# Performance work log

Hardware: AMD Instinct MI355X
Metric: run time of the kernel (lower is better)

## Reference

```python
import jax, jax.numpy as jnp
import numpy as np

# 256 graphs x 1024 nodes, 64 channels, 4.19M edges (avg degree 16)
B, N, C, E = 256, 1024, 64, 4194304
RATIO = 0.5
K = 512  # ceil(RATIO * N), fixed per-graph keep count


def setup_inputs() -> dict:
    key = jax.random.key(0)
    k1, k2, k3, k4, k5, k6 = jax.random.split(key, 6)
    x = jax.random.normal(k1, (B * N, C), jnp.float32)
    w = jax.random.normal(k2, (1, C), jnp.float32) / np.sqrt(C)  # score_layer.weight
    b = jnp.zeros((1,), jnp.float32)                              # score_layer.bias
    # edges sampled within each graph so filter_adj semantics are realistic
    g = jax.random.randint(k3, (E,), 0, B)
    src = jax.random.randint(k4, (E,), 0, N)
    dst = jax.random.randint(k5, (E,), 0, N)
    edge_index = jnp.stack([g * N + src, g * N + dst]).astype(jnp.int32)
    edge_attr = jax.random.normal(k6, (E,), jnp.float32)
    batch = jnp.repeat(jnp.arange(B, dtype=jnp.int32), N)  # nondecreasing graph ids
    return {"x": x, "w": w, "b": b, "edge_index": edge_index,
            "edge_attr": edge_attr, "batch": batch}


def reference(x, w, b, edge_index, edge_attr, batch):
    # scores = Linear(x).squeeze() / ||W||  (bias also divided, as in source)
    scores = (x @ w.T + b)[:, 0] / jnp.linalg.norm(w)  # [B*N]
    # per-graph ratio top-k (equal-size graphs -> dense [B, N] top_k, fixed K)
    _, top_idx = jax.lax.top_k(scores.reshape(B, N), K)          # [B, K] local ids
    perm = (top_idx + (jnp.arange(B) * N)[:, None]).reshape(-1)  # [B*K] global ids
    x_p = x[perm]          # gather surviving node features
    batch_p = batch[perm]
    # filter_adj: relabel kept nodes 0..B*K-1, drop edges touching removed nodes.
    # For jit-able static shapes we keep [2, E] and mask dropped edges to -1
    # instead of compacting (mask returned for downstream compaction).
    new_idx = jnp.full((B * N,), -1, jnp.int32).at[perm].set(
        jnp.arange(B * K, dtype=jnp.int32))
    r = new_idx[edge_index[0]]
    c = new_idx[edge_index[1]]
    mask = (r >= 0) & (c >= 0)
    ei = jnp.where(mask, jnp.stack([r, c]), -1)
    ea = jnp.where(mask, edge_attr, jnp.zeros((), edge_attr.dtype))
    return x_p, ei, ea, batch_p, scores, perm, mask
```

## Files before the change

### kernel.cpp

```cpp
#include <hip/hip_runtime.h>
#include <math.h>

#define BGRAPHS 256
#define NNODES  1024
#define CCH     64
#define NEDGE   4194304
#define KKEEP   512

typedef unsigned long long u64;
typedef unsigned int u32;
typedef unsigned short u16;
typedef float  f32x4 __attribute__((ext_vector_type(4)));
typedef int    i32x4 __attribute__((ext_vector_type(4)));

#define OFF_XP   0
#define OFF_EI0  8388608
#define OFF_EI1  (8388608 + NEDGE)
#define OFF_EA   16777216
#define OFF_BP   20971520
#define OFF_SC   21102592
#define OFF_PM   21364736
#define OFF_MSK  21495808

#define EDGE_BLOCKS   2048
#define GATHER_BLOCKS 8192

__global__ __launch_bounds__(256) void score_kernel(
    const float* __restrict__ x, const float* __restrict__ w,
    const float* __restrict__ bias, float* __restrict__ sco)
{
    __shared__ float s_w[CCH];
    const int tid = threadIdx.x;
    if (tid < CCH) s_w[tid] = w[tid];
    __syncthreads();

    double n2 = 0.0;
    #pragma unroll
    for (int k = 0; k < CCH; ++k) { double v = (double)s_w[k]; n2 += v * v; }
    const float nrm = (float)sqrt(n2);
    const float bv = bias[0];

    const int node = blockIdx.x * 256 + tid;
    const f32x4* x4 = (const f32x4*)x;
    double acc = 0.0;
    #pragma unroll
    for (int k = 0; k < 16; ++k) {
        f32x4 xv = x4[node * 16 + k];
        acc += (double)xv.x * (double)s_w[4 * k + 0];
        acc += (double)xv.y * (double)s_w[4 * k + 1];
        acc += (double)xv.z * (double)s_w[4 * k + 2];
        acc += (double)xv.w * (double)s_w[4 * k + 3];
    }
    sco[node] = ((float)acc + bv) / nrm;
}

__device__ __forceinline__ u64 cmpex(u64 key, int j, bool dir, int tid) {
    u64 o = (u64)__shfl_xor((long long)key, j, 64);
    bool lower = ((tid & j) == 0);
    u64 mn = key < o ? key : o;
    u64 mx = key < o ? o : key;
    return (dir == lower) ? mn : mx;
}

__global__ __launch_bounds__(1024) void sort_kernel(
    const float* __restrict__ sco, const int* __restrict__ batch,
    float* __restrict__ pmo, float* __restrict__ bpo,
    u16* __restrict__ table16, u16* __restrict__ src16)
{
    __shared__ u64 s_key[NNODES];
    const int b = blockIdx.x;
    const int tid = threadIdx.x;
    const int node = b * NNODES + tid;

    const float score = sco[node];
    u32 u = __float_as_uint(score);
    u32 mu = u ^ (u32)(((int)u >> 31) | 0x80000000);
    u64 key = ((u64)(~mu) << 32) | (u32)tid;

    #pragma unroll
    for (int k = 2; k <= 64; k <<= 1) {
        bool dir = ((tid & k) == 0);
        for (int j = k >> 1; j > 0; j >>= 1)
            key = cmpex(key, j, dir, tid);
    }
    s_key[tid] = key;

    for (int k = 128; k <= NNODES; k <<= 1) {
        bool dir = ((tid & k) == 0);
        for (int j = k >> 1; j >= 64; j >>= 1) {
            __syncthreads();
            int ixj = tid ^ j;
            if (ixj > tid) {
                u64 a = s_key[tid], c = s_key[ixj];
                if ((a > c) == dir) { s_key[tid] = c; s_key[ixj] = a; }
            }
        }
        __syncthreads();
        key = s_key[tid];
        #pragma unroll
        for (int j = 32; j > 0; j >>= 1)
            key = cmpex(key, j, dir, tid);
        s_key[tid] = key;
    }

    const int lidx = (int)(u32)key;
    const int g = b * NNODES + lidx;
    if (tid < KKEEP) {
        pmo[b * KKEEP + tid] = (float)g;
        bpo[b * KKEEP + tid] = (float)batch[g];
        table16[g] = (u16)tid;
        src16[b * KKEEP + tid] = (u16)lidx;
    } else {
        table16[g] = 0xFFFFu;
    }
}

__global__ __launch_bounds__(256) void edge_gather_kernel(
    const int* __restrict__ ei, const float* __restrict__ ea,
    const u16* __restrict__ table16,
    const float* __restrict__ x, const u16* __restrict__ src16,
    float* __restrict__ ei0o, float* __restrict__ ei1o,
    float* __restrict__ eao, float* __restrict__ msk,
    float* __restrict__ xp)
{
    const int tid = threadIdx.x;
    if (blockIdx.x < EDGE_BLOCKS) {
        const int i0 = blockIdx.x * 512 + tid;
        const int i1 = i0 + 256;
        const i32x4* s4p = (const i32x4*)ei;
        const i32x4* d4p = (const i32x4*)(ei + NEDGE);
        const f32x4* a4p = (const f32x4*)ea;

        i32x4 sA = __builtin_nontemporal_load(&s4p[i0]);
        i32x4 sB = __builtin_nontemporal_load(&s4p[i1]);
        i32x4 dA = __builtin_nontemporal_load(&d4p[i0]);
        i32x4 dB = __builtin_nontemporal_load(&d4p[i1]);
        f32x4 aA = __builtin_nontemporal_load(&a4p[i0]);
        f32x4 aB = __builtin_nontemporal_load(&a4p[i1]);

        u16 vsA[4], vdA[4], vsB[4], vdB[4];
        #pragma unroll
        for (int q = 0; q < 4; ++q) vsA[q] = table16[((const int*)&sA)[q]];
        #pragma unroll
        for (int q = 0; q < 4; ++q) vdA[q] = table16[((const int*)&dA)[q]];
        #pragma unroll
        for (int q = 0; q < 4; ++q) vsB[q] = table16[((const int*)&sB)[q]];
        #pragma unroll
        for (int q = 0; q < 4; ++q) vdB[q] = table16[((const int*)&dB)[q]];

        f32x4 rA, cA, oA, mA, rB, cB, oB, mB;
        #pragma unroll
        for (int q = 0; q < 4; ++q) {
            {
                int m = (vsA[q] != 0xFFFFu) && (vdA[q] != 0xFFFFu);
                int r = ((((const int*)&sA)[q] >> 10) << 9) + (int)vsA[q];
                int c = ((((const int*)&dA)[q] >> 10) << 9) + (int)vdA[q];
                ((float*)&rA)[q] = m ? (float)r : -1.0f;
                ((float*)&cA)[q] = m ? (float)c : -1.0f;
                ((float*)&oA)[q] = m ? ((const float*)&aA)[q] : 0.0f;
                ((float*)&mA)[q] = (float)m;
            }
            {
                int m = (vsB[q] != 0xFFFFu) && (vdB[q] != 0xFFFFu);
                int r = ((((const int*)&sB)[q] >> 10) << 9) + (int)vsB[q];
                int c = ((((const int*)&dB)[q] >> 10) << 9) + (int)vdB[q];
                ((float*)&rB)[q] = m ? (float)r : -1.0f;
                ((float*)&cB)[q] = m ? (float)c : -1.0f;
                ((float*)&oB)[q] = m ? ((const float*)&aB)[q] : 0.0f;
                ((float*)&mB)[q] = (float)m;
            }
        }

        __builtin_nontemporal_store(rA, &((f32x4*)ei0o)[i0]);
        __builtin_nontemporal_store(rB, &((f32x4*)ei0o)[i1]);
        __builtin_nontemporal_store(cA, &((f32x4*)ei1o)[i0]);
        __builtin_nontemporal_store(cB, &((f32x4*)ei1o)[i1]);
        __builtin_nontemporal_store(oA, &((f32x4*)eao)[i0]);
        __builtin_nontemporal_store(oB, &((f32x4*)eao)[i1]);
        __builtin_nontemporal_store(mA, &((f32x4*)msk)[i0]);
        __builtin_nontemporal_store(mB, &((f32x4*)msk)[i1]);
    } else {
        const int elem = (blockIdx.x - EDGE_BLOCKS) * 256 + tid;
        const int row = elem >> 4;
        const int col = elem & 15;
        const int b = row >> 9;
        const int src = (int)src16[row];
        const f32x4* x4 = (const f32x4*)x;
        ((f32x4*)xp)[elem] = x4[((b << 10) + src) * 16 + col];
    }
}

extern "C" void kernel_launch(void* const* d_in, const int* in_sizes, int n_in,
                              void* d_out, int out_size, void* d_ws, size_t ws_size,
                              hipStream_t stream) {
    const float* x          = (const float*)d_in[0];
    const float* w          = (const float*)d_in[1];
    const float* bias       = (const float*)d_in[2];
    const int*   edge_index = (const int*)d_in[3];
    const float* edge_attr  = (const float*)d_in[4];
    const int*   batch      = (const int*)d_in[5];

    float* out = (float*)d_out;
    float* xp   = out + OFF_XP;
    float* ei0o = out + OFF_EI0;
    float* ei1o = out + OFF_EI1;
    float* eao  = out + OFF_EA;
    float* bpo  = out + OFF_BP;
    float* sco  = out + OFF_SC;
    float* pmo  = out + OFF_PM;
    float* msk  = out + OFF_MSK;

    u16* table16 = (u16*)d_ws;
    u16* src16   = (u16*)d_ws + BGRAPHS * NNODES;

    score_kernel<<<BGRAPHS * NNODES / 256, 256, 0, stream>>>(x, w, bias, sco);
    sort_kernel<<<BGRAPHS, 1024, 0, stream>>>(sco, batch, pmo, bpo, table16, src16);
    edge_gather_kernel<<<EDGE_BLOCKS + GATHER_BLOCKS, 256, 0, stream>>>(
        edge_index, edge_attr, table16, x, src16, ei0o, ei1o, eao, msk, xp);
}
```

Before: 244.8 us.

## Fuse edge filtering and feature gather into every thread of one grid

Previously the kernel split blocks into edge-filter blocks and separate gather blocks. Now every thread of a 2048-block grid does its edge work and also gathers four x_p vectors strided by the total thread count. The gather stores also become nontemporal. The aim is more memory-level parallelism per thread and fewer tiny gather blocks, at the cost of higher register pressure and possibly lower occupancy.

```diff
diff --git a/kernel.cpp b/kernel.cpp
--- a/kernel.cpp
+++ b/kernel.cpp
@@ -22,8 +22,8 @@
 #define OFF_PM   21364736
 #define OFF_MSK  21495808
 
-#define EDGE_BLOCKS   2048
-#define GATHER_BLOCKS 8192
+#define FUSED_BLOCKS 2048
+#define GTHREADS     524288
 
 __global__ __launch_bounds__(256) void score_kernel(
     const float* __restrict__ x, const float* __restrict__ w,
@@ -124,70 +124,83 @@
     float* __restrict__ xp)
 {
     const int tid = threadIdx.x;
-    if (blockIdx.x < EDGE_BLOCKS) {
-        const int i0 = blockIdx.x * 512 + tid;
-        const int i1 = i0 + 256;
-        const i32x4* s4p = (const i32x4*)ei;
-        const i32x4* d4p = (const i32x4*)(ei + NEDGE);
-        const f32x4* a4p = (const f32x4*)ea;
-
-        i32x4 sA = __builtin_nontemporal_load(&s4p[i0]);
-        i32x4 sB = __builtin_nontemporal_load(&s4p[i1]);
-        i32x4 dA = __builtin_nontemporal_load(&d4p[i0]);
-        i32x4 dB = __builtin_nontemporal_load(&d4p[i1]);
-        f32x4 aA = __builtin_nontemporal_load(&a4p[i0]);
-        f32x4 aB = __builtin_nontemporal_load(&a4p[i1]);
-
-        u16 vsA[4], vdA[4], vsB[4], vdB[4];
-        #pragma unroll
-        for (int q = 0; q < 4; ++q) vsA[q] = table16[((const int*)&sA)[q]];
-        #pragma unroll
-        for (int q = 0; q < 4; ++q) vdA[q] = table16[((const int*)&dA)[q]];
-        #pragma unroll
-        for (int q = 0; q < 4; ++q) vsB[q] = table16[((const int*)&sB)[q]];
-        #pragma unroll
-        for (int q = 0; q < 4; ++q) vdB[q] = table16[((const int*)&dB)[q]];
-
-        f32x4 rA, cA, oA, mA, rB, cB, oB, mB;
-        #pragma unroll
-        for (int q = 0; q < 4; ++q) {
-            {
-                int m = (vsA[q] != 0xFFFFu) && (vdA[q] != 0xFFFFu);
-                int r = ((((const int*)&sA)[q] >> 10) << 9) + (int)vsA[q];
-                int c = ((((const int*)&dA)[q] >> 10) << 9) + (int)vdA[q];
-                ((float*)&rA)[q] = m ? (float)r : -1.0f;
-                ((float*)&cA)[q] = m ? (float)c : -1.0f;
-                ((float*)&oA)[q] = m ? ((const float*)&aA)[q] : 0.0f;
-                ((float*)&mA)[q] = (float)m;
-            }
-            {
-                int m = (vsB[q] != 0xFFFFu) && (vdB[q] != 0xFFFFu);
-                int r = ((((const int*)&sB)[q] >> 10) << 9) + (int)vsB[q];
-                int c = ((((const int*)&dB)[q] >> 10) << 9) + (int)vdB[q];
-                ((float*)&rB)[q] = m ? (float)r : -1.0f;
-                ((float*)&cB)[q] = m ? (float)c : -1.0f;
-                ((float*)&oB)[q] = m ? ((const float*)&aB)[q] : 0.0f;
-                ((float*)&mB)[q] = (float)m;
-            }
+    const int gt = blockIdx.x * 256 + tid;
+    const int i0 = blockIdx.x * 512 + tid;
+    const int i1 = i0 + 256;
+
+    const i32x4* s4p = (const i32x4*)ei;
+    const i32x4* d4p = (const i32x4*)(ei + NEDGE);
+    const f32x4* a4p = (const f32x4*)ea;
+    const f32x4* x4  = (const f32x4*)x;
+
+    i32x4 sA = __builtin_nontemporal_load(&s4p[i0]);
+    i32x4 sB = __builtin_nontemporal_load(&s4p[i1]);
+    i32x4 dA = __builtin_nontemporal_load(&d4p[i0]);
+    i32x4 dB = __builtin_nontemporal_load(&d4p[i1]);
+    f32x4 aA = __builtin_nontemporal_load(&a4p[i0]);
+    f32x4 aB = __builtin_nontemporal_load(&a4p[i1]);
+
+    int rowv[4], colv[4], srcv[4];
+    #pragma unroll
+    for (int p = 0; p < 4; ++p) {
+        int elem = gt + p * GTHREADS;
+        rowv[p] = elem >> 4;
+        colv[p] = elem & 15;
+        srcv[p] = (int)src16[rowv[p]];
+    }
+
+    u16 vsA[4], vdA[4], vsB[4], vdB[4];
+    #pragma unroll
+    for (int q = 0; q < 4; ++q) vsA[q] = table16[((const int*)&sA)[q]];
+    #pragma unroll
+    for (int q = 0; q < 4; ++q) vdA[q] = table16[((const int*)&dA)[q]];
+    #pragma unroll
+    for (int q = 0; q < 4; ++q) vsB[q] = table16[((const int*)&sB)[q]];
+    #pragma unroll
+    for (int q = 0; q < 4; ++q) vdB[q] = table16[((const int*)&dB)[q]];
+
+    f32x4 xv[4];
+    #pragma unroll
+    for (int p = 0; p < 4; ++p) {
+        int b = rowv[p] >> 9;
+        xv[p] = x4[((b << 10) + srcv[p]) * 16 + colv[p]];
+    }
+
+    f32x4 rA, cA, oA, mA, rB, cB, oB, mB;
+    #pragma unroll
+    for (int q = 0; q < 4; ++q) {
+        {
+            int m = (vsA[q] != 0xFFFFu) && (vdA[q] != 0xFFFFu);
+            int r = ((((const int*)&sA)[q] >> 10) << 9) + (int)vsA[q];
+            int c = ((((const int*)&dA)[q] >> 10) << 9) + (int)vdA[q];
+            ((float*)&rA)[q] = m ? (float)r : -1.0f;
+            ((float*)&cA)[q] = m ? (float)c : -1.0f;
+            ((float*)&oA)[q] = m ? ((const float*)&aA)[q] : 0.0f;
+            ((float*)&mA)[q] = (float)m;
         }
-
-        __builtin_nontemporal_store(rA, &((f32x4*)ei0o)[i0]);
-        __builtin_nontemporal_store(rB, &((f32x4*)ei0o)[i1]);
-        __builtin_nontemporal_store(cA, &((f32x4*)ei1o)[i0]);
-        __builtin_nontemporal_store(cB, &((f32x4*)ei1o)[i1]);
-        __builtin_nontemporal_store(oA, &((f32x4*)eao)[i0]);
-        __builtin_nontemporal_store(oB, &((f32x4*)eao)[i1]);
-        __builtin_nontemporal_store(mA, &((f32x4*)msk)[i0]);
-        __builtin_nontemporal_store(mB, &((f32x4*)msk)[i1]);
-    } else {
-        const int elem = (blockIdx.x - EDGE_BLOCKS) * 256 + tid;
-        const int row = elem >> 4;
-        const int col = elem & 15;
-        const int b = row >> 9;
-        const int src = (int)src16[row];
-        const f32x4* x4 = (const f32x4*)x;
-        ((f32x4*)xp)[elem] = x4[((b << 10) + src) * 16 + col];
-    }
+        {
+            int m = (vsB[q] != 0xFFFFu) && (vdB[q] != 0xFFFFu);
+            int r = ((((const int*)&sB)[q] >> 10) << 9) + (int)vsB[q];
+            int c = ((((const int*)&dB)[q] >> 10) << 9) + (int)vdB[q];
+            ((float*)&rB)[q] = m ? (float)r : -1.0f;
+            ((float*)&cB)[q] = m ? (float)c : -1.0f;
+            ((float*)&oB)[q] = m ? ((const float*)&aB)[q] : 0.0f;
+            ((float*)&mB)[q] = (float)m;
+        }
+    }
+
+    __builtin_nontemporal_store(rA, &((f32x4*)ei0o)[i0]);
+    __builtin_nontemporal_store(rB, &((f32x4*)ei0o)[i1]);
+    __builtin_nontemporal_store(cA, &((f32x4*)ei1o)[i0]);
+    __builtin_nontemporal_store(cB, &((f32x4*)ei1o)[i1]);
+    __builtin_nontemporal_store(oA, &((f32x4*)eao)[i0]);
+    __builtin_nontemporal_store(oB, &((f32x4*)eao)[i1]);
+    __builtin_nontemporal_store(mA, &((f32x4*)msk)[i0]);
+    __builtin_nontemporal_store(mB, &((f32x4*)msk)[i1]);
+
+    #pragma unroll
+    for (int p = 0; p < 4; ++p)
+        __builtin_nontemporal_store(xv[p], &((f32x4*)xp)[gt + p * GTHREADS]);
 }
 
 extern "C" void kernel_launch(void* const* d_in, const int* in_sizes, int n_in,
@@ -215,6 +228,6 @@
 
     score_kernel<<<BGRAPHS * NNODES / 256, 256, 0, stream>>>(x, w, bias, sco);
     sort_kernel<<<BGRAPHS, 1024, 0, stream>>>(sco, batch, pmo, bpo, table16, src16);
-    edge_gather_kernel<<<EDGE_BLOCKS + GATHER_BLOCKS, 256, 0, stream>>>(
+    edge_gather_kernel<<<FUSED_BLOCKS, 256, 0, stream>>>(
         edge_index, edge_attr, table16, x, src16, ei0o, ei1o, eao, msk, xp);
 }
```

Result: faster. 237.8 us (-2.9%).
